# Kernel tuning notes

Hardware: AMD Instinct MI355X
Metric: run time of the kernel (lower is better)

## Reference

```python
import jax, jax.numpy as jnp
import numpy as np

N, E, D, NHID, NOUT, G = 100000, 600000, 128, 512, 768, 2048
EPS = 1e-5

def _lin_init(k, fi, fo):
    s = 1.0 / np.sqrt(fi)
    kw, kb = jax.random.split(k)
    W = jax.random.uniform(kw, (fi, fo), jnp.float32, -s, s)
    b = jax.random.uniform(kb, (fo,), jnp.float32, -s, s)
    return W, b

def setup_inputs():
    key = jax.random.key(0)
    ks = jax.random.split(key, 16)
    inp = {}
    inp['x'] = jax.random.normal(ks[0], (N, D), jnp.float32)
    inp['edge_index'] = jax.random.randint(ks[1], (2, E), 0, N, jnp.int32)
    inp['batch'] = jnp.sort(jax.random.randint(ks[2], (N,), 0, G, jnp.int32))
    # 3 GCN layers + GAT attention layer + 4 MLP linears
    inp['W1'], inp['b1'] = _lin_init(ks[3], D, D)
    inp['W2'], inp['b2'] = _lin_init(ks[4], D, D)
    inp['W3'], inp['b3'] = _lin_init(ks[5], D, D)
    inp['Wa'], inp['ba'] = _lin_init(ks[6], D, D)
    ka1, ka2 = jax.random.split(ks[7])
    inp['a_src'] = jax.random.normal(ka1, (D,), jnp.float32) * 0.1
    inp['a_dst'] = jax.random.normal(ka2, (D,), jnp.float32) * 0.1
    # batchnorm affine params (4 BNs)
    for i, nm in enumerate(['g1', 'g2', 'g3', 'ga']):
        inp[nm] = jnp.ones((D,), jnp.float32)
        inp['be' + nm[1:]] = jnp.zeros((D,), jnp.float32)
    inp['Wl1'], inp['bl1'] = _lin_init(ks[8], D, NHID)
    inp['Wl2'], inp['bl2'] = _lin_init(ks[9], NHID, NHID)
    inp['Wl3'], inp['bl3'] = _lin_init(ks[10], NHID, NHID)
    inp['Wl4'], inp['bl4'] = _lin_init(ks[11], NHID, NOUT)
    inp['gln'] = jnp.ones((NOUT,), jnp.float32)
    inp['bln'] = jnp.zeros((NOUT,), jnp.float32)
    return inp

def _bn(x, g, b):
    # training-mode batchnorm over node dim (biased variance, like torch)
    mu = jnp.mean(x, axis=0)
    var = jnp.var(x, axis=0)
    return (x - mu) * jax.lax.rsqrt(var + EPS) * g + b

def _forward(x, edge_index, batch, W1, b1, g1, be1, W2, b2, g2, be2, W3, b3, g3, be3,
             Wa, ba, a_src, a_dst, ga, bea, Wl1, bl1, Wl2, bl2, Wl3, bl3, Wl4, bl4, gln, bln):
    loop = jnp.arange(N, dtype=edge_index.dtype)
    src = jnp.concatenate([edge_index[0], loop])  # [E+N] with self-loops
    dst = jnp.concatenate([edge_index[1], loop])
    deg = jax.ops.segment_sum(jnp.ones_like(dst, jnp.float32), dst, num_segments=N)
    dinv = jax.lax.rsqrt(deg)  # deg >= 1 thanks to self-loops
    norm = (dinv[src] * dinv[dst])[:, None]  # [E+N, 1]

    def gcn(h, W, b):
        h = h @ W
        return jax.ops.segment_sum(h[src] * norm, dst, num_segments=N) + b

    x = jax.nn.relu(_bn(gcn(x, W1, b1), g1, be1)) + x
    x = jax.nn.relu(_bn(gcn(x, W2, b2), g2, be2)) + x
    x = jax.nn.relu(_bn(gcn(x, W3, b3), g3, be3)) + x

    # GATConv, heads=1: edge logit = LeakyReLU(a_src.h_j + a_dst.h_i), softmax over dst
    h = x @ Wa
    al = h @ a_src  # [N]
    ar = h @ a_dst
    e = jax.nn.leaky_relu(al[src] + ar[dst], 0.2)  # [E+N]
    m = jax.ops.segment_max(e, dst, num_segments=N)
    ee = jnp.exp(e - m[dst])
    denom = jax.ops.segment_sum(ee, dst, num_segments=N)
    alpha = (ee / denom[dst])[:, None]
    x = jax.ops.segment_sum(alpha * h[src], dst, num_segments=N) + ba
    x = jax.nn.relu(_bn(x, ga, bea))

    # global_add_pool
    x = jax.ops.segment_sum(x, batch, num_segments=G)  # [G, D]

    x = jax.nn.relu(x @ Wl1 + bl1)
    x = jax.nn.relu(x @ Wl2 + bl2)
    x = jax.nn.relu(x @ Wl3 + bl3)
    x = x @ Wl4 + bl4
    mu = jnp.mean(x, axis=-1, keepdims=True)
    var = jnp.var(x, axis=-1, keepdims=True)
    return (x - mu) * jax.lax.rsqrt(var + EPS) * gln + bln

def reference(x, edge_index, batch, W1, b1, g1, be1, W2, b2, g2, be2, W3, b3, g3, be3,
              Wa, ba, a_src, a_dst, ga, bea, Wl1, bl1, Wl2, bl2, Wl3, bl3, Wl4, bl4, gln, bln):
    return _forward(x, edge_index, batch, W1, b1, g1, be1, W2, b2, g2, be2, W3, b3, g3, be3,
                    Wa, ba, a_src, a_dst, ga, bea, Wl1, bl1, Wl2, bl2, Wl3, bl3, Wl4, bl4, gln, bln)
```

## Files before the change

kernel.cpp:

```cpp
#include <hip/hip_runtime.h>
#include <cstdint>
#include <cstddef>

#define CDIV(a,b) (((a)+(b)-1)/(b))

constexpr int N_ = 100000;
constexpr int E_ = 600000;
constexpr int D_ = 128;
constexpr int G_ = 2048;
constexpr int NHID_ = 512;
constexpr int NOUT_ = 768;
constexpr float EPS_ = 1e-5f;
constexpr int AGG_BLOCKS = 2048;

typedef short bf16x8 __attribute__((ext_vector_type(8)));
typedef float f32x4 __attribute__((ext_vector_type(4)));

__device__ __forceinline__ float wave_sum(float v){
#pragma unroll
  for (int m = 32; m; m >>= 1) v += __shfl_xor(v, m, 64);
  return v;
}
__device__ __forceinline__ float lrelu02(float v){ return v > 0.f ? v : 0.2f * v; }
__device__ __forceinline__ unsigned short f2bf(float f){
  unsigned u = __float_as_uint(f);
  u += 0x7FFF + ((u >> 16) & 1);
  return (unsigned short)(u >> 16);
}
__device__ __forceinline__ float bflo(unsigned u){ return __uint_as_float(u << 16); }
__device__ __forceinline__ float bfhi(unsigned u){ return __uint_as_float(u & 0xFFFF0000u); }

__global__ void k_count(const int* __restrict__ dst, int* __restrict__ cnt){
  int e = blockIdx.x * 256 + threadIdx.x;
  if (e < E_) atomicAdd(&cnt[dst[e]], 1);
}

__global__ void k_dinv(const int* __restrict__ cnt, float* __restrict__ dinv){
  int i = blockIdx.x * 256 + threadIdx.x;
  if (i < N_) dinv[i] = rsqrtf((float)(cnt[i] + 1));
}

__global__ void k_scan1(const int* __restrict__ cnt, int* __restrict__ ro, int* __restrict__ bs){
  __shared__ int s[256];
  int tid = threadIdx.x;
  int i = blockIdx.x * 256 + tid;
  int v = (i < N_) ? cnt[i] : 0;
  s[tid] = v; __syncthreads();
  for (int off = 1; off < 256; off <<= 1){
    int add = (tid >= off) ? s[tid - off] : 0;
    __syncthreads();
    s[tid] += add;
    __syncthreads();
  }
  if (i < N_) ro[i] = s[tid] - v;
  if (tid == 255) bs[blockIdx.x] = s[255];
}

__global__ void k_scan2(int* __restrict__ bs, int nb){
  __shared__ int s[512];
  int t = threadIdx.x;
  int v = (t < nb) ? bs[t] : 0;
  s[t] = v; __syncthreads();
  for (int off = 1; off < 512; off <<= 1){
    int a = (t >= off) ? s[t - off] : 0;
    __syncthreads();
    s[t] += a;
    __syncthreads();
  }
  if (t < nb) bs[t] = s[t] - v;
}

__global__ void k_scan3(int* __restrict__ ro, const int* __restrict__ bs){
  int i = blockIdx.x * 256 + threadIdx.x;
  if (i < N_) ro[i] += bs[i >> 8];
  if (i == N_) ro[N_] = E_;
}

__global__ void k_fill(const int* __restrict__ src, const int* __restrict__ dst,
                       const int* __restrict__ ro, int* __restrict__ cur, int* __restrict__ csr){
  int e = blockIdx.x * 256 + threadIdx.x;
  if (e < E_){
    int d = dst[e];
    int p = atomicAdd(&cur[d], 1);
    csr[ro[d] + p] = src[e];
  }
}

__global__ void k_bounds(const int* __restrict__ batch, int* __restrict__ gs){
  int g = blockIdx.x * 256 + threadIdx.x;
  if (g > G_) return;
  int lo = 0, hi = N_;
  while (lo < hi){ int mid = (lo + hi) >> 1; if (batch[mid] < g) lo = mid + 1; else hi = mid; }
  gs[g] = lo;
}

__global__ void k_wprep(const float* __restrict__ W, short* __restrict__ Wt){
  int i = blockIdx.x * 256 + threadIdx.x;
  if (i >= 128 * 16) return;
  int c = i >> 4, tg = i & 15, t = tg >> 2, g = tg & 3;
  short* o = Wt + (size_t)i * 8;
#pragma unroll
  for (int j = 0; j < 8; ++j){
    int k = t * 32 + (j >> 2) * 16 + g * 4 + (j & 3);
    o[j] = (short)f2bf(W[(size_t)k * 128 + c]);
  }
}

__global__ __launch_bounds__(256) void k_mm_mfma(const float* __restrict__ X,
                                                 const short* __restrict__ Wt,
                                                 unsigned* __restrict__ hout,
                                                 const float* __restrict__ ss,
                                                 const float* __restrict__ res,
                                                 float* __restrict__ xnew,
                                                 const float* __restrict__ prescale,
                                                 const float* __restrict__ asrc,
                                                 const float* __restrict__ adst,
                                                 float* __restrict__ al_out,
                                                 float* __restrict__ ar_out){
  int lane = threadIdx.x & 63, wid = threadIdx.x >> 6;
  int rw0 = blockIdx.x * 64 + wid * 16;
  int cl = lane & 15, g = lane >> 4;
  int arow = rw0 + cl;
  bool rvalid = arow < N_;
  const float4* Xr = (const float4*)(X + (size_t)arow * 128);

  float4 xv[8];
  if (rvalid){
#pragma unroll
    for (int t = 0; t < 4; ++t){
      xv[2*t]   = Xr[t*8 + g];
      xv[2*t+1] = Xr[t*8 + g + 4];
    }
  } else {
#pragma unroll
    for (int i = 0; i < 8; ++i) xv[i] = make_float4(0.f,0.f,0.f,0.f);
  }

  if (ss){
    float4 rv[8];
    if (res && rvalid){
      const float4* Rr = (const float4*)(res + (size_t)arow * 128);
#pragma unroll
      for (int t = 0; t < 4; ++t){
        rv[2*t]   = Rr[t*8 + g];
        rv[2*t+1] = Rr[t*8 + g + 4];
      }
    } else {
#pragma unroll
      for (int i = 0; i < 8; ++i) rv[i] = make_float4(0.f,0.f,0.f,0.f);
    }
#pragma unroll
    for (int t = 0; t < 4; ++t){
      int f0 = t * 32 + g * 4;
#pragma unroll
      for (int h = 0; h < 2; ++h){
        float4 sc = *(const float4*)&ss[f0 + 16*h];
        float4 sh = *(const float4*)&ss[128 + f0 + 16*h];
        float4& v = xv[2*t + h];
        const float4& r = rv[2*t + h];
        v.x = fmaxf(v.x*sc.x+sh.x, 0.f) + r.x;
        v.y = fmaxf(v.y*sc.y+sh.y, 0.f) + r.y;
        v.z = fmaxf(v.z*sc.z+sh.z, 0.f) + r.z;
        v.w = fmaxf(v.w*sc.w+sh.w, 0.f) + r.w;
      }
      if (xnew && rvalid){
        float4* Nw = (float4*)(xnew + (size_t)arow * 128);
        Nw[t*8 + g]     = xv[2*t];
        Nw[t*8 + g + 4] = xv[2*t+1];
      }
    }
  }

  f32x4 acc[8];
#pragma unroll
  for (int j = 0; j < 8; ++j) acc[j] = (f32x4){0.f, 0.f, 0.f, 0.f};

#pragma unroll
  for (int t = 0; t < 4; ++t){
    bf16x8 af;
    const float4& a = xv[2*t];
    const float4& b = xv[2*t+1];
    af[0]=(short)f2bf(a.x); af[1]=(short)f2bf(a.y); af[2]=(short)f2bf(a.z); af[3]=(short)f2bf(a.w);
    af[4]=(short)f2bf(b.x); af[5]=(short)f2bf(b.y); af[6]=(short)f2bf(b.z); af[7]=(short)f2bf(b.w);
#pragma unroll
    for (int j = 0; j < 8; ++j){
      int c = j * 16 + cl;
      bf16x8 bf = *(const bf16x8*)(Wt + ((size_t)c * 16 + t * 4 + g) * 8);
      acc[j] = __builtin_amdgcn_mfma_f32_16x16x32_bf16(af, bf, acc[j], 0, 0, 0);
    }
  }

#pragma unroll
  for (int r = 0; r < 4; ++r){
    int row = rw0 + g * 4 + r;
    if (row < N_){
      float psc = prescale ? prescale[row] : 1.f;
#pragma unroll
      for (int jp = 0; jp < 4; ++jp){
        unsigned lo = f2bf(acc[2*jp][r] * psc);
        unsigned hi = f2bf(acc[2*jp+1][r] * psc);
        hout[(size_t)row * 64 + jp * 16 + cl] = (hi << 16) | lo;
      }
    }
  }

  if (al_out){
    float pal[4] = {0,0,0,0}, par[4] = {0,0,0,0};
#pragma unroll
    for (int j = 0; j < 8; ++j){
      float as_ = asrc[j * 16 + cl], ad_ = adst[j * 16 + cl];
#pragma unroll
      for (int r = 0; r < 4; ++r){ pal[r] += acc[j][r] * as_; par[r] += acc[j][r] * ad_; }
    }
#pragma unroll
    for (int m = 1; m < 16; m <<= 1)
#pragma unroll
      for (int r = 0; r < 4; ++r){
        pal[r] += __shfl_xor(pal[r], m, 64);
        par[r] += __shfl_xor(par[r], m, 64);
      }
    if (cl == 0){
#pragma unroll
      for (int r = 0; r < 4; ++r){
        int row = rw0 + g * 4 + r;
        if (row < N_){ al_out[row] = pal[r]; ar_out[row] = par[r]; }
      }
    }
  }
}

__global__ __launch_bounds__(256) void k_gcn_agg2(const unsigned* __restrict__ hbf, const int* __restrict__ ro,
                          const int* __restrict__ csr, const float* __restrict__ dinv,
                          const float* __restrict__ bias, float* __restrict__ outb,
                          float4* __restrict__ pbuf){
  int wid = threadIdx.x >> 6, lane = threadIdx.x & 63;
  int f0 = 32 * (lane >> 4) + (lane & 15), f1 = f0 + 16;
  float bb0 = bias[f0], bb1 = bias[f1];
  float S0 = 0.f, S1 = 0.f, Q0 = 0.f, Q1 = 0.f;
  for (int node = blockIdx.x * 4 + wid; node < N_; node += AGG_BLOCKS * 4){
    int s0 = ro[node], s1 = ro[node + 1];
    int deg = s1 - s0;
    float di = dinv[node];
    unsigned us = hbf[(size_t)node * 64 + lane];
    float a0 = bflo(us), a1 = bfhi(us);
    if (deg <= 64){
      int sidx = (lane < deg) ? csr[s0 + lane] : 0;
      int j = 0;
      for (; j + 4 <= deg; j += 4){
        int sa = __shfl(sidx, j, 64),   sb = __shfl(sidx, j+1, 64);
        int sc = __shfl(sidx, j+2, 64), sd = __shfl(sidx, j+3, 64);
        unsigned ua = hbf[(size_t)sa*64+lane], ub = hbf[(size_t)sb*64+lane];
        unsigned uc = hbf[(size_t)sc*64+lane], ud = hbf[(size_t)sd*64+lane];
        a0 += bflo(ua) + bflo(ub) + bflo(uc) + bflo(ud);
        a1 += bfhi(ua) + bfhi(ub) + bfhi(uc) + bfhi(ud);
      }
      for (; j < deg; ++j){
        int s = __shfl(sidx, j, 64);
        unsigned u = hbf[(size_t)s*64+lane];
        a0 += bflo(u); a1 += bfhi(u);
      }
    } else {
      for (int base = s0; base < s1; base += 64){
        int c = min(64, s1 - base);
        int sidx = (lane < c) ? csr[base + lane] : 0;
        for (int j = 0; j < c; ++j){
          int s = __shfl(sidx, j, 64);
          unsigned u = hbf[(size_t)s*64+lane];
          a0 += bflo(u); a1 += bfhi(u);
        }
      }
    }
    float o0 = di * a0 + bb0;
    float o1 = di * a1 + bb1;
    outb[(size_t)node * 128 + f0] = o0;
    outb[(size_t)node * 128 + f1] = o1;
    S0 += o0; S1 += o1; Q0 += o0*o0; Q1 += o1*o1;
  }
  __shared__ float4 sred[4][64];
  sred[wid][lane] = make_float4(S0, S1, Q0, Q1);
  __syncthreads();
  if (wid == 0){
    float4 t = sred[0][lane];
    float4 u1 = sred[1][lane], u2 = sred[2][lane], u3 = sred[3][lane];
    t.x += u1.x + u2.x + u3.x;
    t.y += u1.y + u2.y + u3.y;
    t.z += u1.z + u2.z + u3.z;
    t.w += u1.w + u2.w + u3.w;
    pbuf[(size_t)blockIdx.x * 64 + lane] = t;
  }
}

__global__ __launch_bounds__(256) void k_gat_agg2(const unsigned* __restrict__ hbf, const int* __restrict__ ro,
                          const int* __restrict__ csr, const float* __restrict__ al,
                          const float* __restrict__ ar, const float* __restrict__ bias,
                          float* __restrict__ outb, float4* __restrict__ pbuf){
  int wid = threadIdx.x >> 6, lane = threadIdx.x & 63;
  int f0 = 32 * (lane >> 4) + (lane & 15), f1 = f0 + 16;
  float bb0 = bias[f0], bb1 = bias[f1];
  float S0 = 0.f, S1 = 0.f, Q0 = 0.f, Q1 = 0.f;
  for (int node = blockIdx.x * 4 + wid; node < N_; node += AGG_BLOCKS * 4){
    int s0 = ro[node], s1 = ro[node + 1];
    int deg = s1 - s0;
    float ari = ar[node], ali = al[node];
    float pself = __expf(lrelu02(ali + ari));
    unsigned uself = hbf[(size_t)node * 64 + lane];
    float h0 = bflo(uself), h1 = bfhi(uself);
    float a0, a1;
    if (deg <= 64){
      int sidx = 0; float p = 0.f;
      if (lane < deg){ sidx = csr[s0 + lane]; p = __expf(lrelu02(al[sidx] + ari)); }
      float invd = 1.f / (wave_sum(p) + pself);
      float wl = p * invd;
      float wsf = pself * invd;
      a0 = wsf * h0; a1 = wsf * h1;
      int j = 0;
      for (; j + 4 <= deg; j += 4){
        int sa = __shfl(sidx, j, 64),   sb = __shfl(sidx, j+1, 64);
        int sc = __shfl(sidx, j+2, 64), sd = __shfl(sidx, j+3, 64);
        float wa = __shfl(wl, j, 64),   wb = __shfl(wl, j+1, 64);
        float wc = __shfl(wl, j+2, 64), wd = __shfl(wl, j+3, 64);
        unsigned ua = hbf[(size_t)sa*64+lane], ub = hbf[(size_t)sb*64+lane];
        unsigned uc = hbf[(size_t)sc*64+lane], ud = hbf[(size_t)sd*64+lane];
        a0 += wa*bflo(ua) + wb*bflo(ub) + wc*bflo(uc) + wd*bflo(ud);
        a1 += wa*bfhi(ua) + wb*bfhi(ub) + wc*bfhi(uc) + wd*bfhi(ud);
      }
      for (; j < deg; ++j){
        int s = __shfl(sidx, j, 64); float w = __shfl(wl, j, 64);
        unsigned u = hbf[(size_t)s*64+lane];
        a0 += w*bflo(u); a1 += w*bfhi(u);
      }
    } else {
      float denom = pself;
      for (int base = s0; base < s1; base += 64){
        int c = min(64, s1 - base);
        float p = 0.f;
        if (lane < c) p = __expf(lrelu02(al[csr[base + lane]] + ari));
        denom += wave_sum(p);
      }
      float invd = 1.f / denom;
      float wsf = pself * invd;
      a0 = wsf * h0; a1 = wsf * h1;
      for (int base = s0; base < s1; base += 64){
        int c = min(64, s1 - base);
        int sidx = 0; float wl = 0.f;
        if (lane < c){ sidx = csr[base + lane]; wl = __expf(lrelu02(al[sidx] + ari)) * invd; }
        for (int j = 0; j < c; ++j){
          int s = __shfl(sidx, j, 64); float w = __shfl(wl, j, 64);
          unsigned u = hbf[(size_t)s*64+lane];
          a0 += w*bflo(u); a1 += w*bfhi(u);
        }
      }
    }
    float o0 = a0 + bb0, o1 = a1 + bb1;
    outb[(size_t)node * 128 + f0] = o0;
    outb[(size_t)node * 128 + f1] = o1;
    S0 += o0; S1 += o1; Q0 += o0*o0; Q1 += o1*o1;
  }
  __shared__ float4 sred[4][64];
  sred[wid][lane] = make_float4(S0, S1, Q0, Q1);
  __syncthreads();
  if (wid == 0){
    float4 t = sred[0][lane];
    float4 u1 = sred[1][lane], u2 = sred[2][lane], u3 = sred[3][lane];
    t.x += u1.x + u2.x + u3.x;
    t.y += u1.y + u2.y + u3.y;
    t.z += u1.z + u2.z + u3.z;
    t.w += u1.w + u2.w + u3.w;
    pbuf[(size_t)blockIdx.x * 64 + lane] = t;
  }
}

__global__ void k_bn_reduce(const float4* __restrict__ pbuf, const float* __restrict__ g,
                            const float* __restrict__ be, float* __restrict__ ss){
  int c = blockIdx.x;
  int f0 = 32 * (c >> 4) + (c & 15), f1 = f0 + 16;
  float4 a = make_float4(0.f, 0.f, 0.f, 0.f);
  for (int r = threadIdx.x; r < AGG_BLOCKS; r += 256){
    float4 v = pbuf[(size_t)r * 64 + c];
    a.x += v.x; a.y += v.y; a.z += v.z; a.w += v.w;
  }
  __shared__ float4 s[256];
  s[threadIdx.x] = a; __syncthreads();
  for (int off = 128; off; off >>= 1){
    if (threadIdx.x < off){
      float4 o = s[threadIdx.x + off];
      s[threadIdx.x].x += o.x; s[threadIdx.x].y += o.y;
      s[threadIdx.x].z += o.z; s[threadIdx.x].w += o.w;
    }
    __syncthreads();
  }
  if (threadIdx.x == 0){
    float4 t = s[0];
    float inv_n = 1.f / (float)N_;
    float mean0 = t.x * inv_n, mean1 = t.y * inv_n;
    float var0 = fmaxf(t.z * inv_n - mean0 * mean0, 0.f);
    float var1 = fmaxf(t.w * inv_n - mean1 * mean1, 0.f);
    float sc0 = g[f0] * rsqrtf(var0 + EPS_);
    float sc1 = g[f1] * rsqrtf(var1 + EPS_);
    ss[f0] = sc0; ss[f1] = sc1;
    ss[128 + f0] = be[f0] - mean0 * sc0;
    ss[128 + f1] = be[f1] - mean1 * sc1;
  }
}

__global__ void k_pool2(const float* __restrict__ xn, const int* __restrict__ gs,
                        const float* __restrict__ ss, float* __restrict__ pooled){
  int g = blockIdx.x, f = threadIdx.x & 127, half = threadIdx.x >> 7;
  int s = gs[g], e = gs[g + 1];
  float sc = ss[f], sh = ss[128 + f];
  float a = 0.f;
  for (int n = s + half; n < e; n += 2)
    a += fmaxf(xn[(size_t)n * 128 + f] * sc + sh, 0.f);
  __shared__ float red[256];
  red[threadIdx.x] = a; __syncthreads();
  if (half == 0) pooled[(size_t)g * 128 + f] = red[f] + red[128 + f];
}

__global__ __launch_bounds__(256) void k_gemm(const float* __restrict__ A, const float* __restrict__ W,
                                              const float* __restrict__ bias, float* __restrict__ C,
                                              int M, int K, int Nc, int relu){
  __shared__ float As[64][17];
  __shared__ float Ws[16][64];
  int tid = threadIdx.x;
  int ty = tid >> 4, tx = tid & 15;
  int rb = blockIdx.y * 64, cb = blockIdx.x * 64;
  float acc[4][4] = {};
  for (int k0 = 0; k0 < K; k0 += 16){
    {
      int r = tid >> 2, kq = tid & 3;
      float4 v = *(const float4*)&A[(size_t)(rb + r) * K + k0 + kq * 4];
      As[r][kq*4+0] = v.x; As[r][kq*4+1] = v.y; As[r][kq*4+2] = v.z; As[r][kq*4+3] = v.w;
    }
    {
      int kk = tid >> 4, cq = tid & 15;
      float4 v = *(const float4*)&W[(size_t)(k0 + kk) * Nc + cb + cq * 4];
      *(float4*)&Ws[kk][cq * 4] = v;
    }
    __syncthreads();
#pragma unroll
    for (int k = 0; k < 16; ++k){
      float a0 = As[ty*4+0][k], a1 = As[ty*4+1][k], a2 = As[ty*4+2][k], a3 = As[ty*4+3][k];
      float b0 = Ws[k][tx], b1 = Ws[k][tx+16], b2 = Ws[k][tx+32], b3 = Ws[k][tx+48];
      acc[0][0] += a0*b0; acc[0][1] += a0*b1; acc[0][2] += a0*b2; acc[0][3] += a0*b3;
      acc[1][0] += a1*b0; acc[1][1] += a1*b1; acc[1][2] += a1*b2; acc[1][3] += a1*b3;
      acc[2][0] += a2*b0; acc[2][1] += a2*b1; acc[2][2] += a2*b2; acc[2][3] += a2*b3;
      acc[3][0] += a3*b0; acc[3][1] += a3*b1; acc[3][2] += a3*b2; acc[3][3] += a3*b3;
    }
    __syncthreads();
  }
#pragma unroll
  for (int i = 0; i < 4; ++i)
#pragma unroll
    for (int j = 0; j < 4; ++j){
      int c = cb + tx + 16 * j;
      float v = acc[i][j] + bias[c];
      if (relu) v = fmaxf(v, 0.f);
      C[(size_t)(rb + ty*4 + i) * Nc + c] = v;
    }
}

__global__ void k_layernorm(const float* __restrict__ xin, const float* __restrict__ g,
                            const float* __restrict__ b, float* __restrict__ out){
  __shared__ float red[8];
  int row = blockIdx.x, tid = threadIdx.x;
  float v0 = xin[(size_t)row*768 + tid];
  float v1 = xin[(size_t)row*768 + tid + 256];
  float v2 = xin[(size_t)row*768 + tid + 512];
  float s = v0 + v1 + v2;
  float q = v0*v0 + v1*v1 + v2*v2;
  s = wave_sum(s); q = wave_sum(q);
  int wid = tid >> 6;
  if ((tid & 63) == 0){ red[wid] = s; red[4 + wid] = q; }
  __syncthreads();
  if (tid == 0){
    float ts = red[0] + red[1] + red[2] + red[3];
    float tq = red[4] + red[5] + red[6] + red[7];
    float mean = ts / 768.f;
    float var = tq / 768.f - mean * mean;
    red[0] = mean; red[1] = rsqrtf(fmaxf(var, 0.f) + EPS_);
  }
  __syncthreads();
  float mean = red[0], inv = red[1];
  out[(size_t)row*768 + tid]       = (v0 - mean) * inv * g[tid]       + b[tid];
  out[(size_t)row*768 + tid + 256] = (v1 - mean) * inv * g[tid + 256] + b[tid + 256];
  out[(size_t)row*768 + tid + 512] = (v2 - mean) * inv * g[tid + 512] + b[tid + 512];
}

extern "C" void kernel_launch(void* const* d_in, const int* in_sizes, int n_in,
                              void* d_out, int out_size, void* d_ws, size_t ws_size,
                              hipStream_t stream){
  const float* x     = (const float*)d_in[0];
  const int*   ei    = (const int*)d_in[1];
  const int*   src   = ei;
  const int*   dst   = ei + E_;
  const int*   batch = (const int*)d_in[2];
  const float* W1 = (const float*)d_in[3];  const float* b1 = (const float*)d_in[4];
  const float* W2 = (const float*)d_in[5];  const float* b2 = (const float*)d_in[6];
  const float* W3 = (const float*)d_in[7];  const float* b3 = (const float*)d_in[8];
  const float* Wa = (const float*)d_in[9];  const float* ba = (const float*)d_in[10];
  const float* a_src = (const float*)d_in[11]; const float* a_dst = (const float*)d_in[12];
  const float* g1 = (const float*)d_in[13]; const float* be1 = (const float*)d_in[14];
  const float* g2 = (const float*)d_in[15]; const float* be2 = (const float*)d_in[16];
  const float* g3 = (const float*)d_in[17]; const float* be3 = (const float*)d_in[18];
  const float* ga = (const float*)d_in[19]; const float* bea = (const float*)d_in[20];
  const float* Wl1 = (const float*)d_in[21]; const float* bl1 = (const float*)d_in[22];
  const float* Wl2 = (const float*)d_in[23]; const float* bl2 = (const float*)d_in[24];
  const float* Wl3 = (const float*)d_in[25]; const float* bl3 = (const float*)d_in[26];
  const float* Wl4 = (const float*)d_in[27]; const float* bl4 = (const float*)d_in[28];
  const float* gln = (const float*)d_in[29]; const float* bln = (const float*)d_in[30];
  float* out = (float*)d_out;

  char* base = (char*)d_ws;
  size_t off = 0;
  auto alloc = [&](size_t bytes)->char*{
    char* p = base + off;
    off += (bytes + 255) & ~(size_t)255;
    return p;
  };
  int*   cnt    = (int*)  alloc((size_t)N_ * 4);
  float* dinv   = (float*)alloc((size_t)N_ * 4);
  int*   ro     = (int*)  alloc((size_t)(N_ + 1) * 4);
  int*   bs     = (int*)  alloc(512 * 4);
  int*   cur    = (int*)  alloc((size_t)N_ * 4);
  int*   csr    = (int*)  alloc((size_t)E_ * 4);
  int*   gstart = (int*)  alloc((size_t)(G_ + 1) * 4);
  float* al     = (float*)alloc((size_t)N_ * 4);
  float* ar     = (float*)alloc((size_t)N_ * 4);
  float* ss     = (float*)alloc(256 * 4);
  float4* pbuf  = (float4*)alloc((size_t)AGG_BLOCKS * 64 * 16);
  short* wt1    = (short*)alloc((size_t)128 * 128 * 2);
  short* wt2    = (short*)alloc((size_t)128 * 128 * 2);
  short* wt3    = (short*)alloc((size_t)128 * 128 * 2);
  short* wta    = (short*)alloc((size_t)128 * 128 * 2);
  unsigned* bufH= (unsigned*)alloc((size_t)N_ * 64 * 4);
  float* bufY   = (float*)alloc((size_t)N_ * D_ * 4);
  float* xres   = (float*)alloc((size_t)N_ * D_ * 4);
  float* pooled = (float*)alloc((size_t)G_ * D_ * 4);
  float* m1     = (float*)alloc((size_t)G_ * NHID_ * 4);
  float* m2     = (float*)alloc((size_t)G_ * NHID_ * 4);
  float* m4     = (float*)alloc((size_t)G_ * NOUT_ * 4);
  (void)ws_size; (void)in_sizes; (void)n_in; (void)out_size;

  const int nbE = CDIV(E_, 256), nbN = CDIV(N_, 256);
  const int MMB = CDIV(N_, 64);

  hipMemsetAsync(cnt, 0, (size_t)N_ * 4, stream);
  k_count<<<nbE, 256, 0, stream>>>(dst, cnt);
  k_dinv<<<nbN, 256, 0, stream>>>(cnt, dinv);
  k_scan1<<<nbN, 256, 0, stream>>>(cnt, ro, bs);
  k_scan2<<<1, 512, 0, stream>>>(bs, nbN);
  k_scan3<<<CDIV(N_ + 1, 256), 256, 0, stream>>>(ro, bs);
  hipMemsetAsync(cur, 0, (size_t)N_ * 4, stream);
  k_fill<<<nbE, 256, 0, stream>>>(src, dst, ro, cur, csr);
  k_bounds<<<CDIV(G_ + 1, 256), 256, 0, stream>>>(batch, gstart);
  k_wprep<<<8, 256, 0, stream>>>(W1, wt1);
  k_wprep<<<8, 256, 0, stream>>>(W2, wt2);
  k_wprep<<<8, 256, 0, stream>>>(W3, wt3);
  k_wprep<<<8, 256, 0, stream>>>(Wa, wta);

  k_mm_mfma<<<MMB, 256, 0, stream>>>(x, wt1, bufH, nullptr, nullptr, nullptr,
                                     dinv, nullptr, nullptr, nullptr, nullptr);
  k_gcn_agg2<<<AGG_BLOCKS, 256, 0, stream>>>(bufH, ro, csr, dinv, b1, bufY, pbuf);
  k_bn_reduce<<<64, 256, 0, stream>>>(pbuf, g1, be1, ss);
  k_mm_mfma<<<MMB, 256, 0, stream>>>(bufY, wt2, bufH, ss, x, xres,
                                     dinv, nullptr, nullptr, nullptr, nullptr);
  k_gcn_agg2<<<AGG_BLOCKS, 256, 0, stream>>>(bufH, ro, csr, dinv, b2, bufY, pbuf);
  k_bn_reduce<<<64, 256, 0, stream>>>(pbuf, g2, be2, ss);
  k_mm_mfma<<<MMB, 256, 0, stream>>>(bufY, wt3, bufH, ss, xres, xres,
                                     dinv, nullptr, nullptr, nullptr, nullptr);
  k_gcn_agg2<<<AGG_BLOCKS, 256, 0, stream>>>(bufH, ro, csr, dinv, b3, bufY, pbuf);
  k_bn_reduce<<<64, 256, 0, stream>>>(pbuf, g3, be3, ss);
  k_mm_mfma<<<MMB, 256, 0, stream>>>(bufY, wta, bufH, ss, xres, nullptr,
                                     nullptr, a_src, a_dst, al, ar);
  k_gat_agg2<<<AGG_BLOCKS, 256, 0, stream>>>(bufH, ro, csr, al, ar, ba, bufY, pbuf);
  k_bn_reduce<<<64, 256, 0, stream>>>(pbuf, ga, bea, ss);
  k_pool2<<<G_, 256, 0, stream>>>(bufY, gstart, ss, pooled);
  k_gemm<<<dim3(NHID_/64, G_/64), 256, 0, stream>>>(pooled, Wl1, bl1, m1, G_, D_, NHID_, 1);
  k_gemm<<<dim3(NHID_/64, G_/64), 256, 0, stream>>>(m1, Wl2, bl2, m2, G_, NHID_, NHID_, 1);
  k_gemm<<<dim3(NHID_/64, G_/64), 256, 0, stream>>>(m2, Wl3, bl3, m1, G_, NHID_, NHID_, 1);
  k_gemm<<<dim3(NOUT_/64, G_/64), 256, 0, stream>>>(m1, Wl4, bl4, m4, G_, NHID_, NOUT_, 0);
  k_layernorm<<<G_, 256, 0, stream>>>(m4, gln, bln, out);
}
```

Baseline: 599.6 us.

## Store aggregation outputs and residual in packed bf16, double rows per GEMM wave

The GCN/GAT aggregation outputs and the residual stream are now stored as packed bf16 pairs in the MFMA fragment's lane layout instead of fp32. The node GEMM and pooling read them back through templated load paths. Each GEMM wave also processes two 16-row tiles, reusing each weight fragment load across both. This cuts the bytes moved by the bandwidth-bound N×128 intermediates roughly in half and reduces weight reloads. In exchange, the residual and pre-BN activations lose precision and the GEMM kernel uses more registers.

```diff
diff --git a/kernel.cpp b/kernel.cpp
--- a/kernel.cpp
+++ b/kernel.cpp
@@ -29,6 +29,30 @@
 }
 __device__ __forceinline__ float bflo(unsigned u){ return __uint_as_float(u << 16); }
 __device__ __forceinline__ float bfhi(unsigned u){ return __uint_as_float(u & 0xFFFF0000u); }
+
+__device__ __forceinline__ float4 unplo(uint4 u){ return make_float4(bflo(u.x), bflo(u.y), bflo(u.z), bflo(u.w)); }
+__device__ __forceinline__ float4 unphi(uint4 u){ return make_float4(bfhi(u.x), bfhi(u.y), bfhi(u.z), bfhi(u.w)); }
+__device__ __forceinline__ float4 bnrelu4(float4 v, float4 sc, float4 sh){
+  return make_float4(fmaxf(v.x*sc.x+sh.x, 0.f), fmaxf(v.y*sc.y+sh.y, 0.f),
+                     fmaxf(v.z*sc.z+sh.z, 0.f), fmaxf(v.w*sc.w+sh.w, 0.f));
+}
+__device__ __forceinline__ float4 add4(float4 a, float4 b){
+  return make_float4(a.x+b.x, a.y+b.y, a.z+b.z, a.w+b.w);
+}
+__device__ __forceinline__ uint4 pk4(float4 lo, float4 hi){
+  uint4 u;
+  u.x = (unsigned)f2bf(lo.x) | ((unsigned)f2bf(hi.x) << 16);
+  u.y = (unsigned)f2bf(lo.y) | ((unsigned)f2bf(hi.y) << 16);
+  u.z = (unsigned)f2bf(lo.z) | ((unsigned)f2bf(hi.z) << 16);
+  u.w = (unsigned)f2bf(lo.w) | ((unsigned)f2bf(hi.w) << 16);
+  return u;
+}
+__device__ __forceinline__ bf16x8 mkaf(float4 lo, float4 hi){
+  bf16x8 a;
+  a[0]=(short)f2bf(lo.x); a[1]=(short)f2bf(lo.y); a[2]=(short)f2bf(lo.z); a[3]=(short)f2bf(lo.w);
+  a[4]=(short)f2bf(hi.x); a[5]=(short)f2bf(hi.y); a[6]=(short)f2bf(hi.z); a[7]=(short)f2bf(hi.w);
+  return a;
+}
 
 __global__ void k_count(const int* __restrict__ dst, int* __restrict__ cnt){
   int e = blockIdx.x * 256 + threadIdx.x;
@@ -106,124 +130,162 @@
   }
 }
 
-__global__ __launch_bounds__(256) void k_mm_mfma(const float* __restrict__ X,
+template<bool XB, bool RB>
+__global__ __launch_bounds__(256) void k_mm_mfma(const void* __restrict__ Xin,
                                                  const short* __restrict__ Wt,
                                                  unsigned* __restrict__ hout,
                                                  const float* __restrict__ ss,
-                                                 const float* __restrict__ res,
-                                                 float* __restrict__ xnew,
+                                                 const void* __restrict__ resin,
+                                                 unsigned* __restrict__ xnew,
                                                  const float* __restrict__ prescale,
                                                  const float* __restrict__ asrc,
                                                  const float* __restrict__ adst,
                                                  float* __restrict__ al_out,
                                                  float* __restrict__ ar_out){
   int lane = threadIdx.x & 63, wid = threadIdx.x >> 6;
-  int rw0 = blockIdx.x * 64 + wid * 16;
   int cl = lane & 15, g = lane >> 4;
-  int arow = rw0 + cl;
-  bool rvalid = arow < N_;
-  const float4* Xr = (const float4*)(X + (size_t)arow * 128);
-
-  float4 xv[8];
-  if (rvalid){
+  int r0a = blockIdx.x * 128 + wid * 16;
+  int r0b = r0a + 64;
+  int rowa = r0a + cl, rowb = r0b + cl;
+  bool va_ = rowa < N_, vb_ = rowb < N_;
+  int rma = va_ ? rowa : 0;
+  int rmb = vb_ ? rowb : 0;
+
+  uint4 xua[4], xub[4];
+  float4 xfa[8], xfb[8];
+  uint4 rua[4], rub[4];
+  float4 rfa[8], rfb[8];
+  bool has_res = resin != nullptr;
+  if (XB){
+    const uint4* Xa = (const uint4*)((const unsigned*)Xin + (size_t)rma * 64);
+    const uint4* Xb = (const uint4*)((const unsigned*)Xin + (size_t)rmb * 64);
+#pragma unroll
+    for (int t = 0; t < 4; ++t){ xua[t] = Xa[t*4 + g]; xub[t] = Xb[t*4 + g]; }
+  } else {
+    const float4* Xa = (const float4*)((const float*)Xin + (size_t)rma * 128);
+    const float4* Xb = (const float4*)((const float*)Xin + (size_t)rmb * 128);
 #pragma unroll
     for (int t = 0; t < 4; ++t){
-      xv[2*t]   = Xr[t*8 + g];
-      xv[2*t+1] = Xr[t*8 + g + 4];
-    }
-  } else {
-#pragma unroll
-    for (int i = 0; i < 8; ++i) xv[i] = make_float4(0.f,0.f,0.f,0.f);
-  }
-
-  if (ss){
-    float4 rv[8];
-    if (res && rvalid){
-      const float4* Rr = (const float4*)(res + (size_t)arow * 128);
+      xfa[2*t] = Xa[t*8 + g]; xfa[2*t+1] = Xa[t*8 + g + 4];
+      xfb[2*t] = Xb[t*8 + g]; xfb[2*t+1] = Xb[t*8 + g + 4];
+    }
+  }
+  if (has_res){
+    if (RB){
+      const uint4* Ra = (const uint4*)((const unsigned*)resin + (size_t)rma * 64);
+      const uint4* Rb = (const uint4*)((const unsigned*)resin + (size_t)rmb * 64);
+#pragma unroll
+      for (int t = 0; t < 4; ++t){ rua[t] = Ra[t*4 + g]; rub[t] = Rb[t*4 + g]; }
+    } else {
+      const float4* Ra = (const float4*)((const float*)resin + (size_t)rma * 128);
+      const float4* Rb = (const float4*)((const float*)resin + (size_t)rmb * 128);
 #pragma unroll
       for (int t = 0; t < 4; ++t){
-        rv[2*t]   = Rr[t*8 + g];
-        rv[2*t+1] = Rr[t*8 + g + 4];
-      }
+        rfa[2*t] = Ra[t*8 + g]; rfa[2*t+1] = Ra[t*8 + g + 4];
+        rfb[2*t] = Rb[t*8 + g]; rfb[2*t+1] = Rb[t*8 + g + 4];
+      }
+    }
+  }
+  __builtin_amdgcn_sched_barrier(0);
+
+  bf16x8 afa[4], afb[4];
+#pragma unroll
+  for (int t = 0; t < 4; ++t){
+    float4 la, ha, lb, hb;
+    if (XB){
+      la = unplo(xua[t]); ha = unphi(xua[t]);
+      lb = unplo(xub[t]); hb = unphi(xub[t]);
     } else {
-#pragma unroll
-      for (int i = 0; i < 8; ++i) rv[i] = make_float4(0.f,0.f,0.f,0.f);
-    }
-#pragma unroll
-    for (int t = 0; t < 4; ++t){
+      la = xfa[2*t]; ha = xfa[2*t+1];
+      lb = xfb[2*t]; hb = xfb[2*t+1];
+    }
+    if (ss){
       int f0 = t * 32 + g * 4;
-#pragma unroll
-      for (int h = 0; h < 2; ++h){
-        float4 sc = *(const float4*)&ss[f0 + 16*h];
-        float4 sh = *(const float4*)&ss[128 + f0 + 16*h];
-        float4& v = xv[2*t + h];
-        const float4& r = rv[2*t + h];
-        v.x = fmaxf(v.x*sc.x+sh.x, 0.f) + r.x;
-        v.y = fmaxf(v.y*sc.y+sh.y, 0.f) + r.y;
-        v.z = fmaxf(v.z*sc.z+sh.z, 0.f) + r.z;
-        v.w = fmaxf(v.w*sc.w+sh.w, 0.f) + r.w;
-      }
-      if (xnew && rvalid){
-        float4* Nw = (float4*)(xnew + (size_t)arow * 128);
-        Nw[t*8 + g]     = xv[2*t];
-        Nw[t*8 + g + 4] = xv[2*t+1];
-      }
-    }
-  }
-
-  f32x4 acc[8];
-#pragma unroll
-  for (int j = 0; j < 8; ++j) acc[j] = (f32x4){0.f, 0.f, 0.f, 0.f};
-
+      float4 sc0 = *(const float4*)&ss[f0],      sh0 = *(const float4*)&ss[128 + f0];
+      float4 sc1 = *(const float4*)&ss[f0 + 16], sh1 = *(const float4*)&ss[128 + f0 + 16];
+      la = bnrelu4(la, sc0, sh0); ha = bnrelu4(ha, sc1, sh1);
+      lb = bnrelu4(lb, sc0, sh0); hb = bnrelu4(hb, sc1, sh1);
+      if (has_res){
+        if (RB){
+          la = add4(la, unplo(rua[t])); ha = add4(ha, unphi(rua[t]));
+          lb = add4(lb, unplo(rub[t])); hb = add4(hb, unphi(rub[t]));
+        } else {
+          la = add4(la, rfa[2*t]); ha = add4(ha, rfa[2*t+1]);
+          lb = add4(lb, rfb[2*t]); hb = add4(hb, rfb[2*t+1]);
+        }
+      }
+      if (xnew){
+        if (va_) *(uint4*)(xnew + (size_t)rowa * 64 + t*16 + g*4) = pk4(la, ha);
+        if (vb_) *(uint4*)(xnew + (size_t)rowb * 64 + t*16 + g*4) = pk4(lb, hb);
+      }
+    }
+    afa[t] = mkaf(la, ha);
+    afb[t] = mkaf(lb, hb);
+  }
+
+  f32x4 accA[8], accB[8];
+#pragma unroll
+  for (int j = 0; j < 8; ++j){ accA[j] = (f32x4){0,0,0,0}; accB[j] = (f32x4){0,0,0,0}; }
 #pragma unroll
   for (int t = 0; t < 4; ++t){
-    bf16x8 af;
-    const float4& a = xv[2*t];
-    const float4& b = xv[2*t+1];
-    af[0]=(short)f2bf(a.x); af[1]=(short)f2bf(a.y); af[2]=(short)f2bf(a.z); af[3]=(short)f2bf(a.w);
-    af[4]=(short)f2bf(b.x); af[5]=(short)f2bf(b.y); af[6]=(short)f2bf(b.z); af[7]=(short)f2bf(b.w);
 #pragma unroll
     for (int j = 0; j < 8; ++j){
       int c = j * 16 + cl;
       bf16x8 bf = *(const bf16x8*)(Wt + ((size_t)c * 16 + t * 4 + g) * 8);
-      acc[j] = __builtin_amdgcn_mfma_f32_16x16x32_bf16(af, bf, acc[j], 0, 0, 0);
+      accA[j] = __builtin_amdgcn_mfma_f32_16x16x32_bf16(afa[t], bf, accA[j], 0, 0, 0);
+      accB[j] = __builtin_amdgcn_mfma_f32_16x16x32_bf16(afb[t], bf, accB[j], 0, 0, 0);
     }
   }
 
 #pragma unroll
   for (int r = 0; r < 4; ++r){
-    int row = rw0 + g * 4 + r;
-    if (row < N_){
-      float psc = prescale ? prescale[row] : 1.f;
+    int ra = r0a + g * 4 + r;
+    if (ra < N_){
+      float psc = prescale ? prescale[ra] : 1.f;
 #pragma unroll
       for (int jp = 0; jp < 4; ++jp){
-        unsigned lo = f2bf(acc[2*jp][r] * psc);
-        unsigned hi = f2bf(acc[2*jp+1][r] * psc);
-        hout[(size_t)row * 64 + jp * 16 + cl] = (hi << 16) | lo;
+        unsigned lo = f2bf(accA[2*jp][r] * psc);
+        unsigned hi = f2bf(accA[2*jp+1][r] * psc);
+        hout[(size_t)ra * 64 + jp * 16 + cl] = (hi << 16) | lo;
+      }
+    }
+    int rb = r0b + g * 4 + r;
+    if (rb < N_){
+      float psc = prescale ? prescale[rb] : 1.f;
+#pragma unroll
+      for (int jp = 0; jp < 4; ++jp){
+        unsigned lo = f2bf(accB[2*jp][r] * psc);
+        unsigned hi = f2bf(accB[2*jp+1][r] * psc);
+        hout[(size_t)rb * 64 + jp * 16 + cl] = (hi << 16) | lo;
       }
     }
   }
 
   if (al_out){
-    float pal[4] = {0,0,0,0}, par[4] = {0,0,0,0};
+    float pal[8] = {0,0,0,0,0,0,0,0}, par[8] = {0,0,0,0,0,0,0,0};
 #pragma unroll
     for (int j = 0; j < 8; ++j){
       float as_ = asrc[j * 16 + cl], ad_ = adst[j * 16 + cl];
 #pragma unroll
-      for (int r = 0; r < 4; ++r){ pal[r] += acc[j][r] * as_; par[r] += acc[j][r] * ad_; }
+      for (int r = 0; r < 4; ++r){
+        pal[r]   += accA[j][r] * as_; par[r]   += accA[j][r] * ad_;
+        pal[4+r] += accB[j][r] * as_; par[4+r] += accB[j][r] * ad_;
+      }
     }
 #pragma unroll
     for (int m = 1; m < 16; m <<= 1)
 #pragma unroll
-      for (int r = 0; r < 4; ++r){
+      for (int r = 0; r < 8; ++r){
         pal[r] += __shfl_xor(pal[r], m, 64);
         par[r] += __shfl_xor(par[r], m, 64);
       }
     if (cl == 0){
 #pragma unroll
       for (int r = 0; r < 4; ++r){
-        int row = rw0 + g * 4 + r;
-        if (row < N_){ al_out[row] = pal[r]; ar_out[row] = par[r]; }
+        int ra = r0a + g * 4 + r;
+        if (ra < N_){ al_out[ra] = pal[r]; ar_out[ra] = par[r]; }
+        int rb = r0b + g * 4 + r;
+        if (rb < N_){ al_out[rb] = pal[4+r]; ar_out[rb] = par[4+r]; }
       }
     }
   }
@@ -231,7 +293,7 @@
 
 __global__ __launch_bounds__(256) void k_gcn_agg2(const unsigned* __restrict__ hbf, const int* __restrict__ ro,
                           const int* __restrict__ csr, const float* __restrict__ dinv,
-                          const float* __restrict__ bias, float* __restrict__ outb,
+                          const float* __restrict__ bias, unsigned* __restrict__ outb,
                           float4* __restrict__ pbuf){
   int wid = threadIdx.x >> 6, lane = threadIdx.x & 63;
   int f0 = 32 * (lane >> 4) + (lane & 15), f1 = f0 + 16;
@@ -272,8 +334,7 @@
     }
     float o0 = di * a0 + bb0;
     float o1 = di * a1 + bb1;
-    outb[(size_t)node * 128 + f0] = o0;
-    outb[(size_t)node * 128 + f1] = o1;
+    outb[(size_t)node * 64 + lane] = (unsigned)f2bf(o0) | ((unsigned)f2bf(o1) << 16);
     S0 += o0; S1 += o1; Q0 += o0*o0; Q1 += o1*o1;
   }
   __shared__ float4 sred[4][64];
@@ -293,7 +354,7 @@
 __global__ __launch_bounds__(256) void k_gat_agg2(const unsigned* __restrict__ hbf, const int* __restrict__ ro,
                           const int* __restrict__ csr, const float* __restrict__ al,
                           const float* __restrict__ ar, const float* __restrict__ bias,
-                          float* __restrict__ outb, float4* __restrict__ pbuf){
+                          unsigned* __restrict__ outb, float4* __restrict__ pbuf){
   int wid = threadIdx.x >> 6, lane = threadIdx.x & 63;
   int f0 = 32 * (lane >> 4) + (lane & 15), f1 = f0 + 16;
   float bb0 = bias[f0], bb1 = bias[f1];
@@ -352,8 +413,7 @@
       }
     }
     float o0 = a0 + bb0, o1 = a1 + bb1;
-    outb[(size_t)node * 128 + f0] = o0;
-    outb[(size_t)node * 128 + f1] = o1;
+    outb[(size_t)node * 64 + lane] = (unsigned)f2bf(o0) | ((unsigned)f2bf(o1) << 16);
     S0 += o0; S1 += o1; Q0 += o0*o0; Q1 += o1*o1;
   }
   __shared__ float4 sred[4][64];
@@ -403,17 +463,22 @@
   }
 }
 
-__global__ void k_pool2(const float* __restrict__ xn, const int* __restrict__ gs,
+__global__ void k_pool2(const unsigned* __restrict__ xn, const int* __restrict__ gs,
                         const float* __restrict__ ss, float* __restrict__ pooled){
   int g = blockIdx.x, f = threadIdx.x & 127, half = threadIdx.x >> 7;
+  int idx = ((f >> 5) << 4) | (f & 15);
+  int hi = (f >> 4) & 1;
   int s = gs[g], e = gs[g + 1];
   float sc = ss[f], sh = ss[128 + f];
   float a = 0.f;
-  for (int n = s + half; n < e; n += 2)
-    a += fmaxf(xn[(size_t)n * 128 + f] * sc + sh, 0.f);
+  for (int n = s + half; n < e; n += 2){
+    unsigned u = xn[(size_t)n * 64 + idx];
+    float v = hi ? bfhi(u) : bflo(u);
+    a += fmaxf(v * sc + sh, 0.f);
+  }
   __shared__ float red[256];
   red[threadIdx.x] = a; __syncthreads();
-  if (half == 0) pooled[(size_t)g * 128 + f] = red[f] + red[128 + f];
+  if (half == 0) pooled[(size_t)g * 128 + f] = red[threadIdx.x] + red[threadIdx.x + 128];
 }
 
 __global__ __launch_bounds__(256) void k_gemm(const float* __restrict__ A, const float* __restrict__ W,
@@ -532,9 +597,9 @@
   short* wt2    = (short*)alloc((size_t)128 * 128 * 2);
   short* wt3    = (short*)alloc((size_t)128 * 128 * 2);
   short* wta    = (short*)alloc((size_t)128 * 128 * 2);
-  unsigned* bufH= (unsigned*)alloc((size_t)N_ * 64 * 4);
-  float* bufY   = (float*)alloc((size_t)N_ * D_ * 4);
-  float* xres   = (float*)alloc((size_t)N_ * D_ * 4);
+  unsigned* bufH  = (unsigned*)alloc((size_t)N_ * 64 * 4);
+  unsigned* bufYb = (unsigned*)alloc((size_t)N_ * 64 * 4);
+  unsigned* xresb = (unsigned*)alloc((size_t)N_ * 64 * 4);
   float* pooled = (float*)alloc((size_t)G_ * D_ * 4);
   float* m1     = (float*)alloc((size_t)G_ * NHID_ * 4);
   float* m2     = (float*)alloc((size_t)G_ * NHID_ * 4);
@@ -542,7 +607,7 @@
   (void)ws_size; (void)in_sizes; (void)n_in; (void)out_size;
 
   const int nbE = CDIV(E_, 256), nbN = CDIV(N_, 256);
-  const int MMB = CDIV(N_, 64);
+  const int MMB = CDIV(N_, 128);
 
   hipMemsetAsync(cnt, 0, (size_t)N_ * 4, stream);
   k_count<<<nbE, 256, 0, stream>>>(dst, cnt);
@@ -558,23 +623,23 @@
   k_wprep<<<8, 256, 0, stream>>>(W3, wt3);
   k_wprep<<<8, 256, 0, stream>>>(Wa, wta);
 
-  k_mm_mfma<<<MMB, 256, 0, stream>>>(x, wt1, bufH, nullptr, nullptr, nullptr,
-                                     dinv, nullptr, nullptr, nullptr, nullptr);
-  k_gcn_agg2<<<AGG_BLOCKS, 256, 0, stream>>>(bufH, ro, csr, dinv, b1, bufY, pbuf);
+  k_mm_mfma<false,false><<<MMB, 256, 0, stream>>>(x, wt1, bufH, nullptr, nullptr, nullptr,
+                                                  dinv, nullptr, nullptr, nullptr, nullptr);
+  k_gcn_agg2<<<AGG_BLOCKS, 256, 0, stream>>>(bufH, ro, csr, dinv, b1, bufYb, pbuf);
   k_bn_reduce<<<64, 256, 0, stream>>>(pbuf, g1, be1, ss);
-  k_mm_mfma<<<MMB, 256, 0, stream>>>(bufY, wt2, bufH, ss, x, xres,
-                                     dinv, nullptr, nullptr, nullptr, nullptr);
-  k_gcn_agg2<<<AGG_BLOCKS, 256, 0, stream>>>(bufH, ro, csr, dinv, b2, bufY, pbuf);
+  k_mm_mfma<true,false><<<MMB, 256, 0, stream>>>(bufYb, wt2, bufH, ss, x, xresb,
+                                                 dinv, nullptr, nullptr, nullptr, nullptr);
+  k_gcn_agg2<<<AGG_BLOCKS, 256, 0, stream>>>(bufH, ro, csr, dinv, b2, bufYb, pbuf);
   k_bn_reduce<<<64, 256, 0, stream>>>(pbuf, g2, be2, ss);
-  k_mm_mfma<<<MMB, 256, 0, stream>>>(bufY, wt3, bufH, ss, xres, xres,
-                                     dinv, nullptr, nullptr, nullptr, nullptr);
-  k_gcn_agg2<<<AGG_BLOCKS, 256, 0, stream>>>(bufH, ro, csr, dinv, b3, bufY, pbuf);
+  k_mm_mfma<true,true><<<MMB, 256, 0, stream>>>(bufYb, wt3, bufH, ss, xresb, xresb,
+                                                dinv, nullptr, nullptr, nullptr, nullptr);
+  k_gcn_agg2<<<AGG_BLOCKS, 256, 0, stream>>>(bufH, ro, csr, dinv, b3, bufYb, pbuf);
   k_bn_reduce<<<64, 256, 0, stream>>>(pbuf, g3, be3, ss);
-  k_mm_mfma<<<MMB, 256, 0, stream>>>(bufY, wta, bufH, ss, xres, nullptr,
-                                     nullptr, a_src, a_dst, al, ar);
-  k_gat_agg2<<<AGG_BLOCKS, 256, 0, stream>>>(bufH, ro, csr, al, ar, ba, bufY, pbuf);
+  k_mm_mfma<true,true><<<MMB, 256, 0, stream>>>(bufYb, wta, bufH, ss, xresb, nullptr,
+                                                nullptr, a_src, a_dst, al, ar);
+  k_gat_agg2<<<AGG_BLOCKS, 256, 0, stream>>>(bufH, ro, csr, al, ar, ba, bufYb, pbuf);
   k_bn_reduce<<<64, 256, 0, stream>>>(pbuf, ga, bea, ss);
-  k_pool2<<<G_, 256, 0, stream>>>(bufY, gstart, ss, pooled);
+  k_pool2<<<G_, 256, 0, stream>>>(bufYb, gstart, ss, pooled);
   k_gemm<<<dim3(NHID_/64, G_/64), 256, 0, stream>>>(pooled, Wl1, bl1, m1, G_, D_, NHID_, 1);
   k_gemm<<<dim3(NHID_/64, G_/64), 256, 0, stream>>>(m1, Wl2, bl2, m2, G_, NHID_, NHID_, 1);
   k_gemm<<<dim3(NHID_/64, G_/64), 256, 0, stream>>>(m2, Wl3, bl3, m1, G_, NHID_, NHID_, 1);
```

Result: faster. 556.8 us (-7.1%).
